# Kernel optimization log

Measured on AMD Instinct MI355X. Metric: run time of the kernel, lower is better.

## Reference

```python
import jax, jax.numpy as jnp
import numpy as np

EPS = 1e-12

def l2norm(x):
    return x / jnp.maximum(jnp.linalg.norm(x, axis=-1, keepdims=True), EPS)

def setup_inputs() -> dict:
    key = jax.random.key(0)
    ks = jax.random.split(key, 10)
    B, N, Din, D, P, C = 2, 32768, 768, 512, 16, 2
    return {
        "x_s": jax.random.normal(ks[0], (B, N, Din), jnp.float32),
        "coord_s": jax.random.uniform(ks[1], (B, N, 2), jnp.float32),
        "x_l": jax.random.normal(ks[2], (B, N, Din), jnp.float32),
        "coord_l": jax.random.uniform(ks[3], (B, N, 2), jnp.float32),
        "W_proj": jax.random.normal(ks[4], (Din, D), jnp.float32) / np.sqrt(Din),
        "b_proj": jax.random.normal(ks[5], (D,), jnp.float32) * 0.01,
        "prototypes": jax.random.normal(ks[6], (P, D), jnp.float32),
        "text_low": l2norm(jax.random.normal(ks[7], (C, D), jnp.float32)),
        "text_high": l2norm(jax.random.normal(ks[8], (C, D), jnp.float32)),
        "label": jax.random.randint(ks[9], (B,), 0, C, jnp.int64),
    }

def forward_project(x, W, b):
    # Linear projection to hidden size, then L2 normalize (matches visual.forward_project + F.normalize)
    return l2norm(jnp.einsum('bni,id->bnd', x, W) + b)

def attention_pool(feats, prototypes):
    # feats: [B,N,D], prototypes: [P,D]
    D = feats.shape[-1]
    p = l2norm(prototypes)
    scores = jnp.einsum('bnd,pd->bpn', feats, p) / jnp.sqrt(jnp.asarray(D, feats.dtype))
    w = jax.nn.softmax(scores, axis=-1)                  # [B,P,N]
    attended = jnp.einsum('bpn,bnd->bpd', w, feats)       # [B,P,D]
    return l2norm(attended.mean(axis=1))                  # [B,D]

def reference(x_s, coord_s, x_l, coord_l, W_proj, b_proj, prototypes, text_low, text_high, label):
    x_s_proj = forward_project(x_s, W_proj, b_proj)
    x_l_proj = forward_project(x_l, W_proj, b_proj)
    feat_low = attention_pool(x_s_proj, prototypes)
    feat_high = attention_pool(x_l_proj, prototypes)
    logits = feat_low @ text_low.T + feat_high @ text_high.T   # [B,C]
    logp = jax.nn.log_softmax(logits, axis=-1)
    loss = -jnp.mean(jnp.take_along_axis(logp, label[:, None], axis=1))
    Y_prob = jax.nn.softmax(logits, axis=1)
    Y_hat = jnp.argmax(Y_prob, axis=1)
    return Y_prob, Y_hat, loss
```

## Files before the change

### kernel.cpp

```cpp
#include <hip/hip_runtime.h>
#include <math.h>

#define BB   2
#define NN   32768
#define DIN  768
#define DD   512
#define PP   16
#define MTOT (BB*NN)
#define MALL (2*MTOT)
#define NCHUNK 128
#define CHUNK  (NN/NCHUNK)
#define SCALE_INV_SQRT_D 0.04419417382415922f

typedef unsigned short u16;
typedef __attribute__((ext_vector_type(8))) short bf16x8;
typedef __attribute__((ext_vector_type(4))) float f32x4;

#define MFMA(a,b,c) __builtin_amdgcn_mfma_f32_16x16x32_bf16((a),(b),(c),0,0,0)

__device__ __forceinline__ unsigned pack2bf(float a, float b) {
  union { float f; unsigned u; } x{a}, y{b};
  unsigned ra = (x.u + 0x7FFFu + ((x.u >> 16) & 1u)) >> 16;
  unsigned rb = (y.u + 0x7FFFu + ((y.u >> 16) & 1u)) >> 16;
  return ra | (rb << 16);
}
__device__ __forceinline__ u16 f2bf(float a) {
  union { float f; unsigned u; } x{a};
  return (u16)((x.u + 0x7FFFu + ((x.u >> 16) & 1u)) >> 16);
}
__device__ __forceinline__ float bf2f(u16 u) {
  union { unsigned u; float f; } x; x.u = ((unsigned)u) << 16; return x.f;
}

__device__ __forceinline__ float block_reduce_sum_256(float v, float* sred) {
  #pragma unroll
  for (int off = 32; off; off >>= 1) v += __shfl_down(v, off);
  const int lane = threadIdx.x & 63, w = threadIdx.x >> 6;
  if (lane == 0) sred[w] = v;
  __syncthreads();
  float r = sred[0] + sred[1] + sred[2] + sred[3];
  __syncthreads();
  return r;
}

__global__ __launch_bounds__(64) void pre_kernel(
    const float* __restrict__ W, const float* __restrict__ prot,
    const float* __restrict__ bias, uint4* __restrict__ Bf,
    uint4* __restrict__ Wpnb, float* __restrict__ bpn) {
  const int bid = blockIdx.x;
  const int lane = threadIdx.x;
  if (bid < 768) {
    const int nf = bid / 24, ks = bid % 24;
    const int n = nf*16 + (lane & 15);
    const int kb = ks*32 + (lane >> 4)*8;
    unsigned r0 = pack2bf(W[(size_t)(kb+0)*DD + n], W[(size_t)(kb+1)*DD + n]);
    unsigned r1 = pack2bf(W[(size_t)(kb+2)*DD + n], W[(size_t)(kb+3)*DD + n]);
    unsigned r2 = pack2bf(W[(size_t)(kb+4)*DD + n], W[(size_t)(kb+5)*DD + n]);
    unsigned r3 = pack2bf(W[(size_t)(kb+6)*DD + n], W[(size_t)(kb+7)*DD + n]);
    Bf[(size_t)bid*64 + lane] = make_uint4(r0, r1, r2, r3);
    return;
  }
  const int ks = bid - 768;
  const int p = lane & 15, seg = lane >> 4;
  float ssq = 0.f;
  for (int d = seg*128; d < seg*128 + 128; d += 4) {
    float4 v = *(const float4*)&prot[p*DD + d];
    ssq += v.x*v.x + v.y*v.y + v.z*v.z + v.w*v.w;
  }
  ssq += __shfl_xor(ssq, 16);
  ssq += __shfl_xor(ssq, 32);
  const float rnp = 1.f / fmaxf(sqrtf(ssq), 1e-12f);
  if (ks < 24) {
    float v[8];
    #pragma unroll
    for (int j = 0; j < 8; ++j) {
      const int k = ks*32 + seg*8 + j;
      const float* wr = W + (size_t)k * DD;
      const float* pr = prot + p * DD;
      float s = 0.f;
      for (int d = 0; d < DD; d += 4) {
        float4 a = *(const float4*)(wr + d);
        float4 b = *(const float4*)(pr + d);
        s += a.x*b.x + a.y*b.y + a.z*b.z + a.w*b.w;
      }
      v[j] = s * rnp;
    }
    Wpnb[ks*64 + lane] = make_uint4(pack2bf(v[0],v[1]), pack2bf(v[2],v[3]),
                                    pack2bf(v[4],v[5]), pack2bf(v[6],v[7]));
  } else {
    float s = 0.f;
    for (int d = seg*128; d < seg*128 + 128; ++d) s += bias[d] * prot[p*DD + d];
    s += __shfl_xor(s, 16);
    s += __shfl_xor(s, 32);
    if (lane < 16) bpn[lane] = s * rnp;
  }
}

__global__ __launch_bounds__(512, 2) void gemm_kernel(
    const float* __restrict__ Xs, const float* __restrict__ Xl,
    const uint4* __restrict__ Bf, const uint4* __restrict__ Wpnb,
    const float* __restrict__ bias, const float* __restrict__ bpn,
    u16* __restrict__ proj, u16* __restrict__ wbufe,
    float* __restrict__ rnormb, float* __restrict__ espart) {
  __shared__ __align__(16) unsigned char lds[147456];
  const int t = threadIdx.x, lane = t & 63, wid = t >> 6;
  const int wm = wid >> 2, wn = wid & 3;
  const int cl = lane & 15, cg = lane >> 4;
  const int m0g = blockIdx.x * 128;
  const float* Xb = (m0g < MTOT) ? Xs : Xl;
  const int m0l = m0g & (MTOT - 1);
  const int r = t >> 2, c4 = t & 3;
  const float* gA = Xb + (size_t)(m0l + r) * DIN + c4 * 4;
  int wslot[4];
  #pragma unroll
  for (int q = 0; q < 4; ++q)
    wslot[q] = (((r>>4)*2 + (q>>1))*64 + ((q&1)*2 + (c4>>1))*16 + (r&15)) * 16 + (c4&1)*8;

  const bool do_score = (wn == 0);
  f32x4 acc[4][8] = {};
  f32x4 sacc[4] = {};

#define STAGE_B(ktx, buf) \
  { _Pragma("unroll") \
    for (int q_ = 0; q_ < 8; ++q_) { \
      const int c_ = q_*8 + wid; \
      const uint4* src_ = Bf + ((size_t)((c_>>1)*24 + (ktx)*2 + (c_&1)))*64 + lane; \
      __builtin_amdgcn_global_load_lds( \
          (const __attribute__((address_space(1))) void*)src_, \
          (__attribute__((address_space(3))) void*)(lds + 16384 + (buf)*65536 + c_*1024 + lane*16), \
          16, 0, 0); \
    } }

  {
    STAGE_B(0, 0);
    float4 va[4];
    #pragma unroll
    for (int q = 0; q < 4; ++q) va[q] = *(const float4*)(gA + q*16);
    #pragma unroll
    for (int q = 0; q < 4; ++q)
      *(uint2*)(&lds[wslot[q]]) =
          make_uint2(pack2bf(va[q].x, va[q].y), pack2bf(va[q].z, va[q].w));
    __syncthreads();
  }
  int cur = 0;
  for (int kt = 0; kt < 12; ++kt) {
    float4 va[4];
    if (kt < 11) {
      STAGE_B(kt + 1, cur ^ 1);
      #pragma unroll
      for (int q = 0; q < 4; ++q) va[q] = *(const float4*)(gA + (kt+1)*64 + q*16);
    }
    const unsigned char* Bb = lds + 16384 + cur*65536;
    #pragma unroll
    for (int ksl = 0; ksl < 2; ++ksl) {
      bf16x8 af[4], bfr[8];
      #pragma unroll
      for (int i = 0; i < 4; ++i)
        af[i] = *(const bf16x8*)(&lds[(((wm*4 + i)*2 + ksl)*64 + lane)*16]);
      #pragma unroll
      for (int j = 0; j < 8; ++j)
        bfr[j] = *(const bf16x8*)(Bb + ((((wn*8 + j)<<1) | ksl)*64 + lane)*16);
      #pragma unroll
      for (int j = 0; j < 8; ++j)
        #pragma unroll
        for (int m = 0; m < 4; ++m)
          acc[m][j] = MFMA(af[m], bfr[j], acc[m][j]);
      if (do_score) {
        bf16x8 wf = *(const bf16x8*)(Wpnb + (kt*2 + ksl)*64 + lane);
        #pragma unroll
        for (int m = 0; m < 4; ++m) sacc[m] = MFMA(af[m], wf, sacc[m]);
      }
    }
    __syncthreads();
    if (kt < 11) {
      #pragma unroll
      for (int q = 0; q < 4; ++q)
        *(uint2*)(&lds[wslot[q]]) =
            make_uint2(pack2bf(va[q].x, va[q].y), pack2bf(va[q].z, va[q].w));
      __syncthreads();
    }
    cur ^= 1;
  }
#undef STAGE_B
  float* ssqred = (float*)lds;
  float* rnl    = (float*)(lds + 2048);
  float* esp2   = (float*)(lds + 2560);
  u16*   sbuf   = (u16*)  (lds + 2688);
  float bv[8];
  #pragma unroll
  for (int j = 0; j < 8; ++j) bv[j] = bias[wn*128 + j*16 + cl];
  #pragma unroll
  for (int m = 0; m < 4; ++m) {
    #pragma unroll
    for (int rr = 0; rr < 4; ++rr) {
      const int rowl = wm*64 + m*16 + cg*4 + rr;
      u16* pr = proj + (size_t)(m0g + rowl) * DD + wn*128 + cl;
      float sq = 0.f;
      #pragma unroll
      for (int j = 0; j < 8; ++j) {
        float val = acc[m][j][rr] + bv[j];
        pr[j*16] = f2bf(val);
        sq += val * val;
      }
      sq += __shfl_xor(sq, 1); sq += __shfl_xor(sq, 2);
      sq += __shfl_xor(sq, 4); sq += __shfl_xor(sq, 8);
      if (cl == 0) ssqred[rowl*4 + wn] = sq;
    }
  }
  __syncthreads();
  if (t < 128) {
    float ss = ssqred[t*4+0] + ssqred[t*4+1] + ssqred[t*4+2] + ssqred[t*4+3];
    float rn = 1.f / fmaxf(sqrtf(ss), 1e-12f);
    rnl[t] = rn;
    rnormb[m0g + t] = rn;
  }
  __syncthreads();
  if (do_score) {
    const float bpv = bpn[cl];
    float esum = 0.f;
    #pragma unroll
    for (int m = 0; m < 4; ++m)
      #pragma unroll
      for (int rr = 0; rr < 4; ++rr) {
        const int rowl = wm*64 + m*16 + cg*4 + rr;
        const float sc = (sacc[m][rr] + bpv) * rnl[rowl] * SCALE_INV_SQRT_D;
        const float e = expf(sc);
        esum += e;
        sbuf[cl*128 + rowl] = f2bf(e);
      }
    esum += __shfl_xor(esum, 16);
    esum += __shfl_xor(esum, 32);
    if (cg == 0) esp2[wm*16 + cl] = esum;
  }
  __syncthreads();
  if (t < 16) espart[(size_t)blockIdx.x * PP + t] = esp2[t] + esp2[16 + t];
  {
    const int p = t >> 5, i4 = (t & 31) * 4;
    const int sbp = m0g >> 15, nb0 = m0g & (NN - 1);
    *(uint2*)&wbufe[(size_t)(sbp*PP + p) * NN + nb0 + i4] =
        *(const uint2*)&sbuf[p*128 + i4];
  }
}

__global__ __launch_bounds__(256) void isum_kernel(const float* __restrict__ espart,
                                                   float* __restrict__ iSrow) {
  __shared__ float sred[4];
  const int bid = blockIdx.x, sbp = bid >> 4, p = bid & 15;
  const int t = threadIdx.x;
  float s = espart[(size_t)(sbp*256 + t)*PP + p];
  s = block_reduce_sum_256(s, sred);
  if (t == 0) iSrow[bid] = 1.f / s;
}

__global__ __launch_bounds__(256) void attended_kernel(
    const u16* __restrict__ proj, const u16* __restrict__ wbufe,
    const float* __restrict__ rnormb, const float* __restrict__ iSrow,
    float* __restrict__ part) {
  __shared__ float wl[CHUNK];
  __shared__ float iSl[PP];
  const int sb = blockIdx.y, cid = blockIdx.x, t = threadIdx.x;
  const int nbase = cid * CHUNK;
  if (t < PP) iSl[t] = iSrow[sb*PP + t];
  __syncthreads();
  if (t < CHUNK) {
    const int n = nbase + t;
    float s = 0.f;
    #pragma unroll
    for (int p = 0; p < PP; ++p)
      s += bf2f(wbufe[(size_t)(sb*PP + p)*NN + n]) * iSl[p];
    wl[t] = s * rnormb[sb*NN + n] * (1.f / PP);
  }
  __syncthreads();
  float a0 = 0.f, a1 = 0.f;
  const u16* pb = proj + ((size_t)sb * NN + nbase) * DD + 2*t;
  #pragma unroll 8
  for (int n = 0; n < CHUNK; ++n) {
    unsigned uu = *(const unsigned*)(pb + (size_t)n * DD);
    float w = wl[n];
    a0 += w * bf2f((u16)uu);
    a1 += w * bf2f((u16)(uu >> 16));
  }
  *(float2*)&part[((size_t)(sb*NCHUNK + cid))*DD + 2*t] = make_float2(a0, a1);
}

__global__ __launch_bounds__(256) void featred_kernel(
    const float* __restrict__ part, float* __restrict__ fraw) {
  __shared__ float red[2][128];
  const int sb = blockIdx.y, d0 = blockIdx.x * 128, t = threadIdx.x;
  const int dl = t & 127, half = t >> 7;
  float s = 0.f;
  for (int c = half*64; c < half*64 + 64; ++c)
    s += part[((size_t)(sb*NCHUNK + c))*DD + d0 + dl];
  red[half][dl] = s;
  __syncthreads();
  if (t < 128) fraw[sb*DD + d0 + t] = red[0][t] + red[1][t];
}

__global__ __launch_bounds__(256) void final_kernel(
    const float* __restrict__ fraw, const float* __restrict__ textL,
    const float* __restrict__ textH, const int* __restrict__ label,
    float* __restrict__ out) {
  __shared__ float sred[4];
  const int t = threadIdx.x;
  const float* frawL = fraw;
  const float* frawH = fraw + 2*DD;
  float invL[2], invH[2];
  #pragma unroll
  for (int b = 0; b < 2; ++b) {
    float v = 0.f;
    for (int d = t; d < DD; d += 256) { float x = frawL[b*DD + d]; v += x*x; }
    float ss = block_reduce_sum_256(v, sred);
    invL[b] = 1.f / fmaxf(sqrtf(ss), 1e-12f);
    v = 0.f;
    for (int d = t; d < DD; d += 256) { float x = frawH[b*DD + d]; v += x*x; }
    ss = block_reduce_sum_256(v, sred);
    invH[b] = 1.f / fmaxf(sqrtf(ss), 1e-12f);
  }
  float lg[2][2];
  #pragma unroll
  for (int b = 0; b < 2; ++b)
    #pragma unroll
    for (int c = 0; c < 2; ++c) {
      float v = 0.f;
      for (int d = t; d < DD; d += 256)
        v += frawL[b*DD + d] * invL[b] * textL[c*DD + d]
           + frawH[b*DD + d] * invH[b] * textH[c*DD + d];
      lg[b][c] = block_reduce_sum_256(v, sred);
    }
  if (t == 0) {
    float loss = 0.f;
    #pragma unroll
    for (int b = 0; b < 2; ++b) {
      const float m  = fmaxf(lg[b][0], lg[b][1]);
      const float lse = m + logf(expf(lg[b][0]-m) + expf(lg[b][1]-m));
      out[b*2+0] = expf(lg[b][0]-lse); out[b*2+1] = expf(lg[b][1]-lse);
      out[4+b] = (lg[b][1] > lg[b][0]) ? 1.f : 0.f;
      loss += -(lg[b][label[b]] - lse);
    }
    out[6] = loss * 0.5f;
  }
}

extern "C" void kernel_launch(void* const* d_in, const int* in_sizes, int n_in,
                              void* d_out, int out_size, void* d_ws, size_t ws_size,
                              hipStream_t stream) {
  (void)in_sizes; (void)n_in; (void)out_size; (void)ws_size;
  const float* x_s  = (const float*)d_in[0];
  const float* x_l  = (const float*)d_in[2];
  const float* Wp   = (const float*)d_in[4];
  const float* bp   = (const float*)d_in[5];
  const float* prot = (const float*)d_in[6];
  const float* tL   = (const float*)d_in[7];
  const float* tH   = (const float*)d_in[8];
  const int*   label= (const int*)d_in[9];
  float* out = (float*)d_out;

  unsigned char* w8 = (unsigned char*)d_ws;
  u16*   proj   = (u16*)  (w8);
  u16*   wbufe  = (u16*)  (w8 + 134217728);
  float* part   = (float*)(w8 + 138412032);
  float* rnormb = (float*)(w8 + 139460608);
  float* espart = (float*)(w8 + 139984896);
  float* iSrow  = (float*)(w8 + 140050432);
  uint4* Bf     = (uint4*)(w8 + 140051456);
  uint4* Wpnb   = (uint4*)(w8 + 140837888);
  float* bpn    = (float*)(w8 + 140862464);
  float* fraw   = (float*)(w8 + 140863488);

  pre_kernel<<<793, 64, 0, stream>>>(Wp, prot, bp, Bf, Wpnb, bpn);
  gemm_kernel<<<MALL/128, 512, 0, stream>>>(x_s, x_l, Bf, Wpnb, bp, bpn,
                                            proj, wbufe, rnormb, espart);
  isum_kernel<<<64, 256, 0, stream>>>(espart, iSrow);
  attended_kernel<<<dim3(NCHUNK, 4), 256, 0, stream>>>(proj, wbufe, rnormb, iSrow, part);
  featred_kernel<<<dim3(4, 4), 256, 0, stream>>>(part, fraw);
  final_kernel<<<1, 256, 0, stream>>>(fraw, tL, tH, label, out);
}
```

Before: 270.0 us.

## Split prototype scoring out of GEMM into separate kernel and shrink GEMM tile

The fused GEMM used a 128-row tile with 147KB of LDS and extra score MFMAs on one wave column. It now uses a 64-row tile with 73KB of LDS and launch bounds for 4 blocks per CU, plus a K-step of 32 with a single sync per iteration. Prototype scores are computed afterwards by a new scores_kernel that re-reads the bf16 projection and dots it with normalized prototypes. The intent is higher occupancy and a lighter GEMM, at the cost of an extra kernel launch and an extra pass over the 128MB projection buffer. Scores now use the rounded bf16 projection rather than the W·p product, which changes numerics slightly.

Measured after the change: 250.1 us. 1.08x faster.

```diff
diff --git a/kernel.cpp b/kernel.cpp
--- a/kernel.cpp
+++ b/kernel.cpp
@@ -45,8 +45,7 @@
 
 __global__ __launch_bounds__(64) void pre_kernel(
     const float* __restrict__ W, const float* __restrict__ prot,
-    const float* __restrict__ bias, uint4* __restrict__ Bf,
-    uint4* __restrict__ Wpnb, float* __restrict__ bpn) {
+    uint4* __restrict__ Bf, uint4* __restrict__ pnb) {
   const int bid = blockIdx.x;
   const int lane = threadIdx.x;
   if (bid < 768) {
@@ -70,175 +69,148 @@
   ssq += __shfl_xor(ssq, 16);
   ssq += __shfl_xor(ssq, 32);
   const float rnp = 1.f / fmaxf(sqrtf(ssq), 1e-12f);
-  if (ks < 24) {
-    float v[8];
-    #pragma unroll
-    for (int j = 0; j < 8; ++j) {
-      const int k = ks*32 + seg*8 + j;
-      const float* wr = W + (size_t)k * DD;
-      const float* pr = prot + p * DD;
-      float s = 0.f;
-      for (int d = 0; d < DD; d += 4) {
-        float4 a = *(const float4*)(wr + d);
-        float4 b = *(const float4*)(pr + d);
-        s += a.x*b.x + a.y*b.y + a.z*b.z + a.w*b.w;
-      }
-      v[j] = s * rnp;
-    }
-    Wpnb[ks*64 + lane] = make_uint4(pack2bf(v[0],v[1]), pack2bf(v[2],v[3]),
-                                    pack2bf(v[4],v[5]), pack2bf(v[6],v[7]));
-  } else {
-    float s = 0.f;
-    for (int d = seg*128; d < seg*128 + 128; ++d) s += bias[d] * prot[p*DD + d];
-    s += __shfl_xor(s, 16);
-    s += __shfl_xor(s, 32);
-    if (lane < 16) bpn[lane] = s * rnp;
-  }
-}
-
-__global__ __launch_bounds__(512, 2) void gemm_kernel(
+  const int kb = ks*32 + seg*8;
+  float v[8];
+  #pragma unroll
+  for (int j = 0; j < 8; ++j) v[j] = prot[p*DD + kb + j] * rnp;
+  pnb[ks*64 + lane] = make_uint4(pack2bf(v[0],v[1]), pack2bf(v[2],v[3]),
+                                 pack2bf(v[4],v[5]), pack2bf(v[6],v[7]));
+}
+
+__global__ __launch_bounds__(512, 4) void gemm_kernel(
     const float* __restrict__ Xs, const float* __restrict__ Xl,
-    const uint4* __restrict__ Bf, const uint4* __restrict__ Wpnb,
-    const float* __restrict__ bias, const float* __restrict__ bpn,
-    u16* __restrict__ proj, u16* __restrict__ wbufe,
-    float* __restrict__ rnormb, float* __restrict__ espart) {
-  __shared__ __align__(16) unsigned char lds[147456];
-  const int t = threadIdx.x, lane = t & 63, wid = t >> 6;
-  const int wm = wid >> 2, wn = wid & 3;
+    const uint4* __restrict__ Bf, const float* __restrict__ bias,
+    u16* __restrict__ proj, float* __restrict__ rnormb) {
+  __shared__ __align__(16) unsigned char lds[73728];
+  const int t = threadIdx.x, lane = t & 63, wn = t >> 6;
   const int cl = lane & 15, cg = lane >> 4;
-  const int m0g = blockIdx.x * 128;
+  const int m0g = blockIdx.x * 64;
   const float* Xb = (m0g < MTOT) ? Xs : Xl;
   const int m0l = m0g & (MTOT - 1);
-  const int r = t >> 2, c4 = t & 3;
+  const int r = t >> 3, c4 = t & 7;
   const float* gA = Xb + (size_t)(m0l + r) * DIN + c4 * 4;
-  int wslot[4];
-  #pragma unroll
-  for (int q = 0; q < 4; ++q)
-    wslot[q] = (((r>>4)*2 + (q>>1))*64 + ((q&1)*2 + (c4>>1))*16 + (r&15)) * 16 + (c4&1)*8;
-
-  const bool do_score = (wn == 0);
-  f32x4 acc[4][8] = {};
-  f32x4 sacc[4] = {};
+  const int awoff = (r >> 4)*1024 + ((r & 15) + 16*(c4 >> 1))*16 + (c4 & 1)*8;
+
+  f32x4 acc[4][4] = {};
 
 #define STAGE_B(ktx, buf) \
   { _Pragma("unroll") \
-    for (int q_ = 0; q_ < 8; ++q_) { \
-      const int c_ = q_*8 + wid; \
-      const uint4* src_ = Bf + ((size_t)((c_>>1)*24 + (ktx)*2 + (c_&1)))*64 + lane; \
+    for (int q_ = 0; q_ < 4; ++q_) { \
+      const int c_ = q_*8 + wn; \
+      const uint4* src_ = Bf + ((size_t)(c_*24 + (ktx)))*64 + lane; \
       __builtin_amdgcn_global_load_lds( \
           (const __attribute__((address_space(1))) void*)src_, \
-          (__attribute__((address_space(3))) void*)(lds + 16384 + (buf)*65536 + c_*1024 + lane*16), \
+          (__attribute__((address_space(3))) void*)(lds + 8192 + (buf)*32768 + c_*1024 + lane*16), \
           16, 0, 0); \
     } }
 
   {
     STAGE_B(0, 0);
-    float4 va[4];
-    #pragma unroll
-    for (int q = 0; q < 4; ++q) va[q] = *(const float4*)(gA + q*16);
-    #pragma unroll
-    for (int q = 0; q < 4; ++q)
-      *(uint2*)(&lds[wslot[q]]) =
-          make_uint2(pack2bf(va[q].x, va[q].y), pack2bf(va[q].z, va[q].w));
+    float4 va = *(const float4*)gA;
+    *(uint2*)(lds + awoff) = make_uint2(pack2bf(va.x, va.y), pack2bf(va.z, va.w));
+  }
+  __syncthreads();
+  for (int kt = 0; kt < 24; ++kt) {
+    const int cur = kt & 1;
+    float4 va;
+    if (kt < 23) {
+      STAGE_B(kt + 1, cur ^ 1);
+      va = *(const float4*)(gA + (kt + 1) * 32);
+    }
+    bf16x8 af[4], bfr[4];
+    #pragma unroll
+    for (int m = 0; m < 4; ++m)
+      af[m] = *(const bf16x8*)(lds + cur*4096 + m*1024 + lane*16);
+    #pragma unroll
+    for (int j = 0; j < 4; ++j)
+      bfr[j] = *(const bf16x8*)(lds + 8192 + cur*32768 + (wn*4 + j)*1024 + lane*16);
+    #pragma unroll
+    for (int j = 0; j < 4; ++j)
+      #pragma unroll
+      for (int m = 0; m < 4; ++m)
+        acc[m][j] = MFMA(af[m], bfr[j], acc[m][j]);
+    if (kt < 23) {
+      *(uint2*)(lds + (cur^1)*4096 + awoff) =
+          make_uint2(pack2bf(va.x, va.y), pack2bf(va.z, va.w));
+    }
     __syncthreads();
-  }
-  int cur = 0;
-  for (int kt = 0; kt < 12; ++kt) {
-    float4 va[4];
-    if (kt < 11) {
-      STAGE_B(kt + 1, cur ^ 1);
-      #pragma unroll
-      for (int q = 0; q < 4; ++q) va[q] = *(const float4*)(gA + (kt+1)*64 + q*16);
-    }
-    const unsigned char* Bb = lds + 16384 + cur*65536;
-    #pragma unroll
-    for (int ksl = 0; ksl < 2; ++ksl) {
-      bf16x8 af[4], bfr[8];
-      #pragma unroll
-      for (int i = 0; i < 4; ++i)
-        af[i] = *(const bf16x8*)(&lds[(((wm*4 + i)*2 + ksl)*64 + lane)*16]);
-      #pragma unroll
-      for (int j = 0; j < 8; ++j)
-        bfr[j] = *(const bf16x8*)(Bb + ((((wn*8 + j)<<1) | ksl)*64 + lane)*16);
-      #pragma unroll
-      for (int j = 0; j < 8; ++j)
-        #pragma unroll
-        for (int m = 0; m < 4; ++m)
-          acc[m][j] = MFMA(af[m], bfr[j], acc[m][j]);
-      if (do_score) {
-        bf16x8 wf = *(const bf16x8*)(Wpnb + (kt*2 + ksl)*64 + lane);
-        #pragma unroll
-        for (int m = 0; m < 4; ++m) sacc[m] = MFMA(af[m], wf, sacc[m]);
-      }
-    }
-    __syncthreads();
-    if (kt < 11) {
-      #pragma unroll
-      for (int q = 0; q < 4; ++q)
-        *(uint2*)(&lds[wslot[q]]) =
-            make_uint2(pack2bf(va[q].x, va[q].y), pack2bf(va[q].z, va[q].w));
-      __syncthreads();
-    }
-    cur ^= 1;
   }
 #undef STAGE_B
   float* ssqred = (float*)lds;
-  float* rnl    = (float*)(lds + 2048);
-  float* esp2   = (float*)(lds + 2560);
-  u16*   sbuf   = (u16*)  (lds + 2688);
-  float bv[8];
-  #pragma unroll
-  for (int j = 0; j < 8; ++j) bv[j] = bias[wn*128 + j*16 + cl];
+  float bv[4];
+  #pragma unroll
+  for (int j = 0; j < 4; ++j) bv[j] = bias[wn*64 + j*16 + cl];
   #pragma unroll
   for (int m = 0; m < 4; ++m) {
     #pragma unroll
     for (int rr = 0; rr < 4; ++rr) {
-      const int rowl = wm*64 + m*16 + cg*4 + rr;
-      u16* pr = proj + (size_t)(m0g + rowl) * DD + wn*128 + cl;
+      const int rowl = m*16 + cg*4 + rr;
+      u16* pr = proj + (size_t)(m0g + rowl) * DD + wn*64 + cl;
       float sq = 0.f;
       #pragma unroll
-      for (int j = 0; j < 8; ++j) {
+      for (int j = 0; j < 4; ++j) {
         float val = acc[m][j][rr] + bv[j];
         pr[j*16] = f2bf(val);
         sq += val * val;
       }
       sq += __shfl_xor(sq, 1); sq += __shfl_xor(sq, 2);
       sq += __shfl_xor(sq, 4); sq += __shfl_xor(sq, 8);
-      if (cl == 0) ssqred[rowl*4 + wn] = sq;
-    }
-  }
-  __syncthreads();
-  if (t < 128) {
-    float ss = ssqred[t*4+0] + ssqred[t*4+1] + ssqred[t*4+2] + ssqred[t*4+3];
-    float rn = 1.f / fmaxf(sqrtf(ss), 1e-12f);
-    rnl[t] = rn;
-    rnormb[m0g + t] = rn;
-  }
-  __syncthreads();
-  if (do_score) {
-    const float bpv = bpn[cl];
-    float esum = 0.f;
-    #pragma unroll
-    for (int m = 0; m < 4; ++m)
-      #pragma unroll
-      for (int rr = 0; rr < 4; ++rr) {
-        const int rowl = wm*64 + m*16 + cg*4 + rr;
-        const float sc = (sacc[m][rr] + bpv) * rnl[rowl] * SCALE_INV_SQRT_D;
-        const float e = expf(sc);
-        esum += e;
-        sbuf[cl*128 + rowl] = f2bf(e);
-      }
-    esum += __shfl_xor(esum, 16);
-    esum += __shfl_xor(esum, 32);
-    if (cg == 0) esp2[wm*16 + cl] = esum;
-  }
-  __syncthreads();
-  if (t < 16) espart[(size_t)blockIdx.x * PP + t] = esp2[t] + esp2[16 + t];
+      if (cl == 0) ssqred[rowl*8 + wn] = sq;
+    }
+  }
+  __syncthreads();
+  if (t < 64) {
+    float ss = 0.f;
+    #pragma unroll
+    for (int w = 0; w < 8; ++w) ss += ssqred[t*8 + w];
+    rnormb[m0g + t] = 1.f / fmaxf(sqrtf(ss), 1e-12f);
+  }
+}
+
+__global__ __launch_bounds__(256) void scores_kernel(
+    const u16* __restrict__ proj, const uint4* __restrict__ pnb,
+    const float* __restrict__ rnormb, u16* __restrict__ wbufe,
+    float* __restrict__ espart) {
+  __shared__ float esp[4][16];
+  __shared__ u16 sbuf[128][18];
+  const int t = threadIdx.x, lane = t & 63, wave = t >> 6;
+  const int cl = lane & 15, cg = lane >> 4;
+  bf16x8 pf[16];
+  #pragma unroll
+  for (int ks = 0; ks < 16; ++ks) pf[ks] = *(const bf16x8*)(pnb + ks*64 + lane);
+  const int row0b = blockIdx.x * 128;
+  float esum = 0.f;
+  #pragma unroll
+  for (int rg = 0; rg < 2; ++rg) {
+    const int row0 = row0b + wave*32 + rg*16;
+    f32x4 sacc = {0.f, 0.f, 0.f, 0.f};
+    #pragma unroll
+    for (int ks = 0; ks < 16; ++ks) {
+      bf16x8 af = *(const bf16x8*)(proj + (size_t)(row0 + cl)*DD + ks*32 + cg*8);
+      sacc = MFMA(af, pf[ks], sacc);
+    }
+    #pragma unroll
+    for (int rr = 0; rr < 4; ++rr) {
+      const int grow = row0 + cg*4 + rr;
+      const float sc = sacc[rr] * rnormb[grow] * SCALE_INV_SQRT_D;
+      const float e = expf(sc);
+      esum += e;
+      sbuf[wave*32 + rg*16 + cg*4 + rr][cl] = f2bf(e);
+    }
+  }
+  esum += __shfl_xor(esum, 16);
+  esum += __shfl_xor(esum, 32);
+  if (lane < 16) esp[wave][lane] = esum;
+  __syncthreads();
+  if (t < 16)
+    espart[(size_t)blockIdx.x * PP + t] = esp[0][t] + esp[1][t] + esp[2][t] + esp[3][t];
   {
-    const int p = t >> 5, i4 = (t & 31) * 4;
-    const int sbp = m0g >> 15, nb0 = m0g & (NN - 1);
-    *(uint2*)&wbufe[(size_t)(sbp*PP + p) * NN + nb0 + i4] =
-        *(const uint2*)&sbuf[p*128 + i4];
+    const int p = t >> 4, i8 = (t & 15) * 8;
+    const int sbp = row0b >> 15, nb0 = row0b & (NN - 1);
+    u16 tmp[8];
+    #pragma unroll
+    for (int k = 0; k < 8; ++k) tmp[k] = sbuf[i8 + k][p];
+    *(uint4*)&wbufe[(size_t)(sbp*PP + p) * NN + nb0 + i8] = *(const uint4*)tmp;
   }
 }
 
@@ -363,13 +335,12 @@
   float* espart = (float*)(w8 + 139984896);
   float* iSrow  = (float*)(w8 + 140050432);
   uint4* Bf     = (uint4*)(w8 + 140051456);
-  uint4* Wpnb   = (uint4*)(w8 + 140837888);
-  float* bpn    = (float*)(w8 + 140862464);
-  float* fraw   = (float*)(w8 + 140863488);
-
-  pre_kernel<<<793, 64, 0, stream>>>(Wp, prot, bp, Bf, Wpnb, bpn);
-  gemm_kernel<<<MALL/128, 512, 0, stream>>>(x_s, x_l, Bf, Wpnb, bp, bpn,
-                                            proj, wbufe, rnormb, espart);
+  uint4* pnb    = (uint4*)(w8 + 140837888);
+  float* fraw   = (float*)(w8 + 140854272);
+
+  pre_kernel<<<784, 64, 0, stream>>>(Wp, prot, Bf, pnb);
+  gemm_kernel<<<MALL/64, 512, 0, stream>>>(x_s, x_l, Bf, bp, proj, rnormb);
+  scores_kernel<<<MALL/128, 256, 0, stream>>>(proj, pnb, rnormb, wbufe, espart);
   isum_kernel<<<64, 256, 0, stream>>>(espart, iSrow);
   attended_kernel<<<dim3(NCHUNK, 4), 256, 0, stream>>>(proj, wbufe, rnormb, iSrow, part);
   featred_kernel<<<dim3(4, 4), 256, 0, stream>>>(part, fraw);
```
